# Kernel tuning notes

Measured on AMD Instinct MI355X. Metric: run time of the kernel, lower is better.

## Reference

```python
import jax, jax.numpy as jnp
import numpy as np

M = 16          # num_of_ferns
K = 10          # bit functions per fern
P = 8           # num_of_active_words
LP = 3          # log2(P)
D_OUT = 64
K_POW2 = 2 ** K


def setup_inputs() -> dict:
    key = jax.random.key(0)
    kb, kw = jax.random.split(key)
    B = jax.random.uniform(kb, (32, M * K, 64, 64), dtype=jnp.float32)   # bit probs in [0,1]
    weights = jax.random.uniform(kw, (M, K_POW2, D_OUT), dtype=jnp.float32)
    bias = jnp.zeros((D_OUT,), jnp.float32)
    return {"B": B, "weights": weights, "bias": bias}


def _fern_it_at(T):
    """Indices/activations of the P most probable words for one fern.
    T: (N,K,H,W) bit probabilities -> IT int32 (N,P,H,W), AT float (N,P,H,W)."""
    N, Kb, H, W = T.shape
    # most probable word: bit k of WB is (T_k >= 0.5)
    TB = (T >= 0.5).astype(jnp.int32)
    pow2 = (2 ** jnp.arange(Kb, dtype=jnp.int32))[None, :, None, None]
    WB = jnp.sum(TB * pow2, axis=1)                          # (N,H,W)
    # confidence product over all K bits
    bsp = jnp.prod(jnp.maximum(T, 1.0 - T), axis=1)          # (N,H,W)
    # pick LP most ambiguous bits (prune_type==2: argmin |T-0.5|, exclude picked)
    BA = jnp.abs(T - 0.5)
    k_range = jnp.arange(Kb)[None, :, None, None]
    ABI, ABA = [], []
    for _ in range(LP):
        a = jnp.argmin(BA, axis=1)                           # (N,H,W)
        ABI.append(a.astype(jnp.int32))
        ABA.append(jnp.take_along_axis(T, a[:, None], axis=1)[:, 0])
        BA = BA + (k_range == a[:, None]).astype(BA.dtype)   # exclude picked bit
    # enumerate P words: bit j of word index p toggles ambiguous bit j
    p_idx = jnp.arange(P, dtype=jnp.int32)
    AT = jnp.ones((N, P, H, W), T.dtype)
    IT = jnp.broadcast_to(WB[:, None], (N, P, H, W))
    bsp = bsp[:, None]                                       # (N,1,H,W)
    full = jnp.int32(K_POW2 - 1)
    for j in range(LP):
        bit = (((p_idx >> j) & 1) == 1)[None, :, None, None]
        aba = ABA[j][:, None]                                # (N,1,H,W)
        AT = AT * jnp.where(bit, aba, 1.0 - aba)
        bsp = bsp / jnp.maximum(aba, 1.0 - aba)              # remove ambiguous-bit confidence
        mask = (jnp.int32(1) << ABI[j])[:, None]
        IT = jnp.where(bit, IT | mask, IT & (mask ^ full))
    return IT, AT * bsp


def reference(B, weights, bias):
    N, MK, H, W = B.shape
    Bf = B.reshape(N, M, K, H, W)
    out = jnp.zeros((N, H, W, D_OUT), B.dtype)
    for m in range(M):  # fixed small structural loop over ferns
        IT, AT = _fern_it_at(Bf[:, m])
        # weighted gather-accumulate == sparse.mm(Votes, weights[m])
        out = out + jnp.einsum('nphw,nphwd->nhwd', AT, weights[m][IT])
    out = out + bias
    return jnp.transpose(out, (0, 3, 1, 2))                  # (N, D_out, H, W)
```

## Files before the change

kernel.cpp:

```cpp
#include <hip/hip_runtime.h>
#include <hip/hip_fp16.h>

#define MF     16
#define PXB    512
#define WHALF_BYTES (1024 * 64 * 2)

typedef const __attribute__((address_space(1))) unsigned gu32_t;
typedef __attribute__((address_space(3))) unsigned lu32_t;

__device__ __forceinline__ void gl_lds16(const void* g, void* l) {
    __builtin_amdgcn_global_load_lds((gu32_t*)g, (lu32_t*)l, 16, 0, 0);
}

__device__ __forceinline__ unsigned h2pack(float a, float b) {
    __half2 h = __floats2half2_rn(a, b);
    return __builtin_bit_cast(unsigned, h);
}

#define PKFMA(D, W, U) \
    asm("v_pk_fma_f16 %0, %1, %2, %0 op_sel:[0,1,0] op_sel_hi:[1,1,1]" \
        : "+v"(D) : "v"(W), "v"(U))
#define PKMUL(D, W, U) \
    asm("v_pk_mul_f16 %0, %1, %2 op_sel:[0,1] op_sel_hi:[1,1]" \
        : "=v"(D) : "v"(W), "v"(U))
#define MIXADD_LO(ACC, P) \
    asm("v_fma_mix_f32 %0, %1, 1.0, %0 op_sel:[0,0,0] op_sel_hi:[1,0,0]" \
        : "+v"(ACC) : "v"(P))
#define MIXADD_HI(ACC, P) \
    asm("v_fma_mix_f32 %0, %1, 1.0, %0 op_sel:[1,0,0] op_sel_hi:[1,0,0]" \
        : "+v"(ACC) : "v"(P))

__global__ void prepack_kernel(const float* __restrict__ Wt, unsigned* __restrict__ wsH) {
    const int q = blockIdx.x * 256 + threadIdx.x;
    const float2 f = ((const float2*)Wt)[q];
    wsH[q] = h2pack(f.x, f.y);
}

template<bool USE_WS>
__global__ __launch_bounds__(1024, 4)
void fern_kernel(const float* __restrict__ B, const float* __restrict__ Wt,
                 const unsigned* __restrict__ wsH,
                 const float* __restrict__ bias, float* __restrict__ out)
{
    __shared__ __align__(16) unsigned lds[36864];
    unsigned* ldsw = lds;
    unsigned* ldsp0 = lds + 32768;
    unsigned* ldsp1 = lds + 34816;

    const int t   = threadIdx.x;
    const int w   = t >> 6;
    const int ln  = t & 63;
    const int px8 = ln >> 3;
    const int cg  = ln & 7;
    const unsigned cg4 = (unsigned)cg << 4;

    const int gbase = blockIdx.x * PXB;
    const int n     = gbase >> 12;
    const int remb  = gbase & 4095;

    float acc[4][8];
#pragma unroll
    for (int r = 0; r < 4; ++r)
#pragma unroll
        for (int c = 0; c < 8; ++c) acc[r][c] = 0.f;

    const float* Bbase = B + (((size_t)n * (MF * 10)) << 12) + remb;

    float T[10];
    if (t < 512) {
        const float* Bm = Bbase + t;
#pragma unroll
        for (int k = 0; k < 10; ++k) T[k] = Bm[(size_t)k << 12];
    }

    for (int m = 0; m < MF; ++m) {
        if (USE_WS) {
            const char* g = (const char*)wsH + (size_t)m * WHALF_BYTES + (w << 10) + (ln << 4);
            char* l = (char*)lds + (w << 10);
#pragma unroll
            for (int i = 0; i < 8; ++i)
                gl_lds16(g + i * 16384, l + i * 16384);
        } else {
            const float4* src4 = (const float4*)(Wt + ((size_t)m << 16));
#pragma unroll
            for (int i = 0; i < 8; ++i) {
                const int j = i * 1024 + t;
                const float4 f0 = src4[2 * j];
                const float4 f1 = src4[2 * j + 1];
                uint4 o;
                o.x = h2pack(f0.x, f0.y);
                o.y = h2pack(f0.z, f0.w);
                o.z = h2pack(f1.x, f1.y);
                o.w = h2pack(f1.z, f1.w);
                *(uint4*)&ldsw[j * 4] = o;
            }
        }

        if (t < 512) {
            float BA[10]; float bsp = 1.f; int wb = 0;
#pragma unroll
            for (int k = 0; k < 10; ++k) {
                wb |= (T[k] >= 0.5f) ? (1 << k) : 0;
                bsp *= fmaxf(T[k], 1.f - T[k]);
                BA[k] = fabsf(T[k] - 0.5f);
            }
            int abi0, abi1, abi2; float aba0, aba1, aba2;
            {
                int bi = 0; float bv = BA[0]; float tv = T[0];
#pragma unroll
                for (int k = 1; k < 10; ++k) if (BA[k] < bv) { bv = BA[k]; bi = k; tv = T[k]; }
                abi0 = bi; aba0 = tv;
#pragma unroll
                for (int k = 0; k < 10; ++k) BA[k] = (k == bi) ? (BA[k] + 1.f) : BA[k];
            }
            {
                int bi = 0; float bv = BA[0]; float tv = T[0];
#pragma unroll
                for (int k = 1; k < 10; ++k) if (BA[k] < bv) { bv = BA[k]; bi = k; tv = T[k]; }
                abi1 = bi; aba1 = tv;
#pragma unroll
                for (int k = 0; k < 10; ++k) BA[k] = (k == bi) ? (BA[k] + 1.f) : BA[k];
            }
            {
                int bi = 0; float bv = BA[0]; float tv = T[0];
#pragma unroll
                for (int k = 1; k < 10; ++k) if (BA[k] < bv) { bv = BA[k]; bi = k; tv = T[k]; }
                abi2 = bi; aba2 = tv;
            }
            const float m0 = fmaxf(aba0, 1.f - aba0);
            const float m1 = fmaxf(aba1, 1.f - aba1);
            const float m2 = fmaxf(aba2, 1.f - aba2);
            const float bspA = bsp * __builtin_amdgcn_rcpf(m0 * m1 * m2);
            const int mk0 = 1 << abi0, mk1 = 1 << abi1, mk2 = 1 << abi2;
            unsigned uu[8];
#pragma unroll
            for (int p = 0; p < 8; ++p) {
                float at = ((p & 1) ? aba0 : (1.f - aba0));
                at      *= ((p & 2) ? aba1 : (1.f - aba1));
                at      *= ((p & 4) ? aba2 : (1.f - aba2));
                at      *= bspA;
                int it = wb;
                it = (p & 1) ? (it | mk0) : (it & ~mk0);
                it = (p & 2) ? (it | mk1) : (it & ~mk1);
                it = (p & 4) ? (it | mk2) : (it & ~mk2);
                uu[p] = ((unsigned)__half_as_ushort(__float2half_rn(at)) << 16)
                      | ((unsigned)it << 4);
            }
            *(uint4*)&ldsp0[t * 4] = make_uint4(uu[0], uu[1], uu[2], uu[3]);
            *(uint4*)&ldsp1[t * 4] = make_uint4(uu[4], uu[5], uu[6], uu[7]);
        }
        __syncthreads();

        if (t < 512 && m + 1 < MF) {
            const float* Bm = Bbase + (((size_t)(m + 1) * 10) << 12) + t;
#pragma unroll
            for (int k = 0; k < 10; ++k) T[k] = Bm[(size_t)k << 12];
        }

#pragma unroll
        for (int r = 0; r < 4; ++r) {
            const int pxl = w * 32 + r * 8 + px8;
            const uint4 pa = *(const uint4*)&ldsp0[pxl * 4];
            const uint4 pb = *(const uint4*)&ldsp1[pxl * 4];
            const unsigned pu[8] = {pa.x, pa.y, pa.z, pa.w, pb.x, pb.y, pb.z, pb.w};
            unsigned a01, a23, a45, a67;
            {
                const unsigned u = pu[0];
                const unsigned boff = ((u & 0x3FF0u) << 3) + cg4;
                const uint4 w4 = *(const uint4*)((const char*)ldsw + boff);
                PKMUL(a01, w4.x, u);
                PKMUL(a23, w4.y, u);
                PKMUL(a45, w4.z, u);
                PKMUL(a67, w4.w, u);
            }
#pragma unroll
            for (int p = 1; p < 8; ++p) {
                const unsigned u = pu[p];
                const unsigned boff = ((u & 0x3FF0u) << 3) + cg4;
                const uint4 w4 = *(const uint4*)((const char*)ldsw + boff);
                PKFMA(a01, w4.x, u);
                PKFMA(a23, w4.y, u);
                PKFMA(a45, w4.z, u);
                PKFMA(a67, w4.w, u);
            }
            MIXADD_LO(acc[r][0], a01); MIXADD_HI(acc[r][1], a01);
            MIXADD_LO(acc[r][2], a23); MIXADD_HI(acc[r][3], a23);
            MIXADD_LO(acc[r][4], a45); MIXADD_HI(acc[r][5], a45);
            MIXADD_LO(acc[r][6], a67); MIXADD_HI(acc[r][7], a67);
        }
        __syncthreads();
    }

    float* ldst = (float*)lds;
#pragma unroll
    for (int r = 0; r < 4; ++r) {
        const int pxl = w * 32 + r * 8 + px8;
#pragma unroll
        for (int c = 0; c < 8; ++c)
            ldst[(cg * 8 + c) * 513 + pxl] = acc[r][c];
    }
    __syncthreads();
    const int tt = t & 511, hh = t >> 9;
    const size_t obase = ((size_t)n << 18) + (size_t)(remb + tt);
#pragma unroll
    for (int d = 0; d < 32; ++d) {
        const int ch = hh * 32 + d;
        out[obase + ((size_t)ch << 12)] = ldst[ch * 513 + tt] + bias[ch];
    }
}

extern "C" void kernel_launch(void* const* d_in, const int* in_sizes, int n_in,
                              void* d_out, int out_size, void* d_ws, size_t ws_size,
                              hipStream_t stream) {
    (void)in_sizes; (void)n_in; (void)out_size;
    const float* B    = (const float*)d_in[0];
    const float* Wt   = (const float*)d_in[1];
    const float* bias = (const float*)d_in[2];
    float* out        = (float*)d_out;

    const size_t need = (size_t)MF * WHALF_BYTES;
    if (ws_size >= need) {
        unsigned* wsH = (unsigned*)d_ws;
        hipLaunchKernelGGL(prepack_kernel, dim3(2048), dim3(256), 0, stream, Wt, wsH);
        hipLaunchKernelGGL((fern_kernel<true>), dim3(256), dim3(1024), 0, stream,
                           B, Wt, wsH, bias, out);
    } else {
        hipLaunchKernelGGL((fern_kernel<false>), dim3(256), dim3(1024), 0, stream,
                           B, Wt, (const unsigned*)nullptr, bias, out);
    }
}
```

Measured before the change: 82.27 us.

## Split output channels across two blocks to halve LDS weight tile

Each block now handles only half of the 64 output channels for its 512 pixels. The prepack is relaid so each fern's half-table is contiguous, which halves the LDS weight footprint and lets occupancy hints rise, and the grid doubles to 512 blocks. The cost is that both halves recompute the fern index/activation math and both reload B, doubling that work and the B traffic. The B prefetch for the next fern is also moved ahead of the barrier.

Result: slower. 100.6 us (+22.2%).

```diff
diff --git a/kernel.cpp b/kernel.cpp
--- a/kernel.cpp
+++ b/kernel.cpp
@@ -3,7 +3,7 @@
 
 #define MF     16
 #define PXB    512
-#define WHALF_BYTES (1024 * 64 * 2)
+#define WS_BYTES (2 * 1024 * 1024)
 
 typedef const __attribute__((address_space(1))) unsigned gu32_t;
 typedef __attribute__((address_space(3))) unsigned lu32_t;
@@ -31,36 +31,44 @@
         : "+v"(ACC) : "v"(P))
 
 __global__ void prepack_kernel(const float* __restrict__ Wt, unsigned* __restrict__ wsH) {
-    const int q = blockIdx.x * 256 + threadIdx.x;
-    const float2 f = ((const float2*)Wt)[q];
+    const int q    = blockIdx.x * 256 + threadIdx.x;
+    const int m    = q >> 15;
+    const int rem  = q & 32767;
+    const int h    = rem >> 14;
+    const int rem2 = rem & 16383;
+    const int row  = rem2 >> 4;
+    const int j    = rem2 & 15;
+    const float2 f = ((const float2*)Wt)[((m << 10) + row) * 32 + h * 16 + j];
     wsH[q] = h2pack(f.x, f.y);
 }
 
 template<bool USE_WS>
-__global__ __launch_bounds__(1024, 4)
+__global__ __launch_bounds__(1024, 8)
 void fern_kernel(const float* __restrict__ B, const float* __restrict__ Wt,
                  const unsigned* __restrict__ wsH,
                  const float* __restrict__ bias, float* __restrict__ out)
 {
-    __shared__ __align__(16) unsigned lds[36864];
-    unsigned* ldsw = lds;
-    unsigned* ldsp0 = lds + 32768;
-    unsigned* ldsp1 = lds + 34816;
-
-    const int t   = threadIdx.x;
-    const int w   = t >> 6;
-    const int ln  = t & 63;
-    const int px8 = ln >> 3;
-    const int cg  = ln & 7;
+    __shared__ __align__(16) unsigned lds[20480];
+    unsigned* ldsw  = lds;
+    unsigned* ldsp0 = lds + 16384;
+    unsigned* ldsp1 = lds + 18432;
+
+    const int t    = threadIdx.x;
+    const int w    = t >> 6;
+    const int ln   = t & 63;
+    const int px16 = ln >> 2;
+    const int cg   = ln & 3;
     const unsigned cg4 = (unsigned)cg << 4;
 
-    const int gbase = blockIdx.x * PXB;
+    const int h     = blockIdx.x & 1;
+    const int chunk = blockIdx.x >> 1;
+    const int gbase = chunk * PXB;
     const int n     = gbase >> 12;
     const int remb  = gbase & 4095;
 
-    float acc[4][8];
-#pragma unroll
-    for (int r = 0; r < 4; ++r)
+    float acc[2][8];
+#pragma unroll
+    for (int r = 0; r < 2; ++r)
 #pragma unroll
         for (int c = 0; c < 8; ++c) acc[r][c] = 0.f;
 
@@ -75,24 +83,27 @@
 
     for (int m = 0; m < MF; ++m) {
         if (USE_WS) {
-            const char* g = (const char*)wsH + (size_t)m * WHALF_BYTES + (w << 10) + (ln << 4);
-            char* l = (char*)lds + (w << 10);
-#pragma unroll
-            for (int i = 0; i < 8; ++i)
-                gl_lds16(g + i * 16384, l + i * 16384);
+            const char* g = (const char*)wsH + ((size_t)(m * 2 + h) << 16)
+                          + (w << 12) + (ln << 4);
+            char* l = (char*)lds + (w << 12);
+#pragma unroll
+            for (int i = 0; i < 4; ++i)
+                gl_lds16(g + i * 1024, l + i * 1024);
         } else {
-            const float4* src4 = (const float4*)(Wt + ((size_t)m << 16));
-#pragma unroll
-            for (int i = 0; i < 8; ++i) {
-                const int j = i * 1024 + t;
-                const float4 f0 = src4[2 * j];
-                const float4 f1 = src4[2 * j + 1];
+            const float* src = Wt + ((size_t)m << 16) + h * 32;
+#pragma unroll
+            for (int i = 0; i < 4; ++i) {
+                const int j16 = i * 1024 + t;
+                const int row = j16 >> 2, cgi = j16 & 3;
+                const float4* s4 = (const float4*)(src + row * 64 + cgi * 8);
+                const float4 f0 = s4[0];
+                const float4 f1 = s4[1];
                 uint4 o;
                 o.x = h2pack(f0.x, f0.y);
                 o.y = h2pack(f0.z, f0.w);
                 o.z = h2pack(f1.x, f1.y);
                 o.w = h2pack(f1.z, f1.w);
-                *(uint4*)&ldsw[j * 4] = o;
+                *(uint4*)&ldsw[j16 * 4] = o;
             }
         }
 
@@ -149,24 +160,24 @@
             *(uint4*)&ldsp0[t * 4] = make_uint4(uu[0], uu[1], uu[2], uu[3]);
             *(uint4*)&ldsp1[t * 4] = make_uint4(uu[4], uu[5], uu[6], uu[7]);
         }
-        __syncthreads();
 
         if (t < 512 && m + 1 < MF) {
             const float* Bm = Bbase + (((size_t)(m + 1) * 10) << 12) + t;
 #pragma unroll
             for (int k = 0; k < 10; ++k) T[k] = Bm[(size_t)k << 12];
         }
-
-#pragma unroll
-        for (int r = 0; r < 4; ++r) {
-            const int pxl = w * 32 + r * 8 + px8;
+        __syncthreads();
+
+#pragma unroll
+        for (int r = 0; r < 2; ++r) {
+            const int pxl = w * 32 + r * 16 + px16;
             const uint4 pa = *(const uint4*)&ldsp0[pxl * 4];
             const uint4 pb = *(const uint4*)&ldsp1[pxl * 4];
             const unsigned pu[8] = {pa.x, pa.y, pa.z, pa.w, pb.x, pb.y, pb.z, pb.w};
             unsigned a01, a23, a45, a67;
             {
                 const unsigned u = pu[0];
-                const unsigned boff = ((u & 0x3FF0u) << 3) + cg4;
+                const unsigned boff = ((u & 0x3FF0u) << 2) + cg4;
                 const uint4 w4 = *(const uint4*)((const char*)ldsw + boff);
                 PKMUL(a01, w4.x, u);
                 PKMUL(a23, w4.y, u);
@@ -176,7 +187,7 @@
 #pragma unroll
             for (int p = 1; p < 8; ++p) {
                 const unsigned u = pu[p];
-                const unsigned boff = ((u & 0x3FF0u) << 3) + cg4;
+                const unsigned boff = ((u & 0x3FF0u) << 2) + cg4;
                 const uint4 w4 = *(const uint4*)((const char*)ldsw + boff);
                 PKFMA(a01, w4.x, u);
                 PKFMA(a23, w4.y, u);
@@ -193,8 +204,8 @@
 
     float* ldst = (float*)lds;
 #pragma unroll
-    for (int r = 0; r < 4; ++r) {
-        const int pxl = w * 32 + r * 8 + px8;
+    for (int r = 0; r < 2; ++r) {
+        const int pxl = w * 32 + r * 16 + px16;
 #pragma unroll
         for (int c = 0; c < 8; ++c)
             ldst[(cg * 8 + c) * 513 + pxl] = acc[r][c];
@@ -203,9 +214,10 @@
     const int tt = t & 511, hh = t >> 9;
     const size_t obase = ((size_t)n << 18) + (size_t)(remb + tt);
 #pragma unroll
-    for (int d = 0; d < 32; ++d) {
-        const int ch = hh * 32 + d;
-        out[obase + ((size_t)ch << 12)] = ldst[ch * 513 + tt] + bias[ch];
+    for (int d = 0; d < 16; ++d) {
+        const int cl = hh * 16 + d;
+        const int ch = h * 32 + cl;
+        out[obase + ((size_t)ch << 12)] = ldst[cl * 513 + tt] + bias[ch];
     }
 }
 
@@ -218,14 +230,13 @@
     const float* bias = (const float*)d_in[2];
     float* out        = (float*)d_out;
 
-    const size_t need = (size_t)MF * WHALF_BYTES;
-    if (ws_size >= need) {
+    if (ws_size >= (size_t)WS_BYTES) {
         unsigned* wsH = (unsigned*)d_ws;
         hipLaunchKernelGGL(prepack_kernel, dim3(2048), dim3(256), 0, stream, Wt, wsH);
-        hipLaunchKernelGGL((fern_kernel<true>), dim3(256), dim3(1024), 0, stream,
+        hipLaunchKernelGGL((fern_kernel<true>), dim3(512), dim3(1024), 0, stream,
                            B, Wt, wsH, bias, out);
     } else {
-        hipLaunchKernelGGL((fern_kernel<false>), dim3(256), dim3(1024), 0, stream,
+        hipLaunchKernelGGL((fern_kernel<false>), dim3(512), dim3(1024), 0, stream,
                            B, Wt, (const unsigned*)nullptr, bias, out);
     }
 }
```
